# Optimization experiments

Measured on AMD Instinct MI355X. Metric: run time of the kernel, lower is better.

## Reference

```python
import jax, jax.numpy as jnp
import numpy as np

B, L, D, H = 8, 1024, 1024, 16
DH = D // H  # dim_per_head = 64
HG = H // 2  # global/local head split


def setup_inputs() -> dict:
    key = jax.random.key(0)
    ks = jax.random.split(key, 10)
    s = 1.0 / np.sqrt(D)
    return {
        "key": jax.random.normal(ks[0], (B, L, D), jnp.float32),
        "value": jax.random.normal(ks[1], (B, L, D), jnp.float32),
        "query": jax.random.normal(ks[2], (B, L, D), jnp.float32),
        "mask": jax.random.bernoulli(ks[3], 0.1, (B, L, L)),
        "additional_mask": jax.random.bernoulli(ks[4], 0.1, (B, L)),
        "Wk": jax.random.normal(ks[5], (D, D), jnp.float32) * s,
        "bk": jnp.zeros((D,), jnp.float32),
        "Wv": jax.random.normal(ks[6], (D, D), jnp.float32) * s,
        "bv": jnp.zeros((D,), jnp.float32),
        "Wq": jax.random.normal(ks[7], (D, D), jnp.float32) * s,
        "bq": jnp.zeros((D,), jnp.float32),
        "Wo": jax.random.normal(ks[8], (D, D), jnp.float32) * s,
        "bo": jnp.zeros((D,), jnp.float32),
    }


def _shape(x):
    # [B, L, D] -> [B, H, L, DH]
    return x.reshape(B, -1, H, DH).transpose(0, 2, 1, 3)


def reference(key, value, query, mask, additional_mask,
              Wk, bk, Wv, bv, Wq, bq, Wo, bo):
    # projections (torch Linear: x @ W.T + b)
    k = _shape(key @ Wk.T + bk)
    v = _shape(value @ Wv.T + bv)
    q = _shape(query @ Wq.T + bq) * (1.0 / np.sqrt(DH))  # scale query (edge_feature=None, additional_mask given)

    qg, ql = q[:, :HG], q[:, HG:]
    kg, kl = k[:, :HG], k[:, HG:]
    vg, vl = v[:, :HG], v[:, HG:]

    # global heads: standard masked attention
    score_g = jnp.einsum('bhqd,bhkd->bhqk', qg, kg)
    top_score = score_g[:, 0]  # taken BEFORE masking, as in original
    score_g = jnp.where(mask[:, None, :, :], -1e18, score_g)
    attn_g = jax.nn.softmax(score_g, axis=-1)  # dropout = identity (eval)
    ctx_g = jnp.einsum('bhqk,bhkd->bhqd', attn_g, vg)

    # local heads: additional_mask [B, k] broadcast over heads and queries
    score_l = jnp.einsum('bhqd,bhkd->bhqk', ql, kl)
    score_l = jnp.where(additional_mask[:, None, None, :], -1e18, score_l)
    attn_l = jax.nn.softmax(score_l, axis=-1)
    ctx_l = jnp.einsum('bhqk,bhkd->bhqd', attn_l, vl)

    ctx = jnp.concatenate([ctx_g, ctx_l], axis=1)          # [B, H, L, DH]
    ctx = ctx.transpose(0, 2, 1, 3).reshape(B, -1, D)      # unshape -> [B, L, D]
    out = ctx @ Wo.T + bo
    return out, top_score
```

## Files before the change

### kernel.cpp

```cpp
#include <hip/hip_runtime.h>
#include <hip/hip_bf16.h>

typedef unsigned short u16;
typedef unsigned int u32;
typedef __attribute__((ext_vector_type(8))) short short8;
typedef __attribute__((ext_vector_type(4))) short short4v;
typedef __attribute__((ext_vector_type(4))) float floatx4;

#define BB 8
#define LL 1024
#define DD 1024
#define HH 16
#define DHH 64
#define NEGBIG (-3.0e38f)
#define QSCALE 0.1803368801111204f
#define LN2F   0.6931471805599453f
#define DEFER_THR 12.0f

__device__ inline u16 f2b(float f) {
  union { __hip_bfloat16 h; u16 u; } cv;
  cv.h = __float2bfloat16(f);
  return cv.u;
}
__device__ inline float b2f(u16 u) {
  union { u16 u; __hip_bfloat16 h; } cv;
  cv.u = u;
  return __bfloat162float(cv.h);
}
__device__ inline float fin(float v, float sentinel) {
  return (fabsf(v) < 1e30f) ? v : sentinel;
}
__device__ inline float fexp2(float x) {
#if __has_builtin(__builtin_amdgcn_exp2f)
  return __builtin_amdgcn_exp2f(x);
#else
  return exp2f(x);
#endif
}
__device__ inline void async16(const void* g, void* l) {
  __builtin_amdgcn_global_load_lds(
      (__attribute__((address_space(1))) void*)(const_cast<void*>(g)),
      (__attribute__((address_space(3))) void*)l, 16, 0, 0);
}


__global__ __launch_bounds__(256) void convpack(
    const float* __restrict__ Wk, const float* __restrict__ Wv,
    const float* __restrict__ Wq, const float* __restrict__ Wo,
    const int* __restrict__ mask, const int* __restrict__ amask,
    u16* __restrict__ Wkb, u16* __restrict__ Wvb, u16* __restrict__ Wqb,
    u16* __restrict__ Wob, u32* __restrict__ maskb, u32* __restrict__ amaskb) {
  const int job = blockIdx.y;
  const int gtid = blockIdx.x * 256 + threadIdx.x;
  const int stride = gridDim.x * 256;

  if (job < 4) {
    const float* src; u16* dst;
    switch (job) {
      case 0: src = Wk; dst = Wkb; break;
      case 1: src = Wv; dst = Wvb; break;
      case 2: src = Wq; dst = Wqb; break;
      default: src = Wo; dst = Wob; break;
    }
    const size_t n4 = (size_t)DD * DD / 4;
    for (size_t i = gtid; i < n4; i += stride) {
      float4 v = ((const float4*)src)[i];
      short4v s;
      s[0] = (short)f2b(v.x); s[1] = (short)f2b(v.y);
      s[2] = (short)f2b(v.z); s[3] = (short)f2b(v.w);
      *(short4v*)(dst + i * 4) = s;
    }
  } else if (job == 4) {
    const size_t nw = (size_t)BB * LL * LL / 32;
    for (size_t w = gtid; w < nw; w += stride) {
      const int4* src = (const int4*)(mask + w * 32);
      u32 bits = 0;
#pragma unroll
      for (int c = 0; c < 8; c++) {
        int4 v = src[c];
        bits |= (u32)(v.x != 0) << (c * 4);
        bits |= (u32)(v.y != 0) << (c * 4 + 1);
        bits |= (u32)(v.z != 0) << (c * 4 + 2);
        bits |= (u32)(v.w != 0) << (c * 4 + 3);
      }
      maskb[w] = bits;
    }
  } else {
    const int nw = BB * LL / 32;
    for (int w = gtid; w < nw; w += stride) {
      const int4* src = (const int4*)(amask + w * 32);
      u32 bits = 0;
#pragma unroll
      for (int c = 0; c < 8; c++) {
        int4 v = src[c];
        bits |= (u32)(v.x != 0) << (c * 4);
        bits |= (u32)(v.y != 0) << (c * 4 + 1);
        bits |= (u32)(v.z != 0) << (c * 4 + 2);
        bits |= (u32)(v.w != 0) << (c * 4 + 3);
      }
      amaskb[w] = bits;
    }
  }
}

__global__ __launch_bounds__(256) void gemm_qkv(
    const float* __restrict__ key, const float* __restrict__ value,
    const float* __restrict__ query, const u16* __restrict__ Wkb,
    const u16* __restrict__ Wvb, const u16* __restrict__ Wqb,
    const float* __restrict__ bk, const float* __restrict__ bv,
    const float* __restrict__ bq, u16* __restrict__ kbuf,
    u16* __restrict__ vbt, u16* __restrict__ qbuf) {
  __shared__ u16 As[2][128 * 32];
  __shared__ u16 Ws[3][128 * 32];

  const int z = blockIdx.z;
  const int tid = threadIdx.x;
  const int wave = tid >> 6, lane = tid & 63;
  const int lr = lane & 15, lq = lane >> 4;
  const int row0 = blockIdx.x * 128;
  const int col0 = blockIdx.y * 128;
  const int wm = (wave & 1) * 64, wn = (wave >> 1) * 64;

  floatx4 acc[4][4];
#pragma unroll
  for (int i = 0; i < 4; i++)
#pragma unroll
    for (int j = 0; j < 4; j++) acc[i][j] = (floatx4){0.f, 0.f, 0.f, 0.f};

  const float* A = (z == 0) ? key : (z == 1) ? value : query;
  const u16* Wb  = (z == 0) ? Wkb : (z == 1) ? Wvb : Wqb;

  const int cc0 = tid, cc1 = 256 + tid;
  const u16* Wg0 = Wb + (size_t)(col0 + (cc0 >> 2)) * 1024 + (cc0 & 3) * 8;
  const u16* Wg1 = Wb + (size_t)(col0 + (cc1 >> 2)) * 1024 + (cc1 & 3) * 8;

  auto stageW = [&](int t, int wbuf) {
    const int o = t * 32;
    async16(Wg0 + o, &Ws[wbuf][wave * 512]);
    async16(Wg1 + o, &Ws[wbuf][2048 + wave * 512]);
  };
  auto loadA = [&](int t, float4* ag) {
#pragma unroll
    for (int it = 0; it < 4; it++) {
      const int cc = it * 256 + tid;
      ag[it] = *(const float4*)(A + (size_t)(row0 + (cc >> 3)) * 1024 +
                                (cc & 7) * 4 + t * 32);
    }
  };
  auto writeA = [&](int abuf, const float4* ag) {
#pragma unroll
    for (int it = 0; it < 4; it++) {
      const int cc = it * 256 + tid;
      short4v s;
      s[0] = (short)f2b(ag[it].x); s[1] = (short)f2b(ag[it].y);
      s[2] = (short)f2b(ag[it].z); s[3] = (short)f2b(ag[it].w);
      *(short4v*)(&As[abuf][(cc >> 3) * 32 + (cc & 7) * 4]) = s;
    }
  };

  float4 ag[3][4];

  stageW(0, 0);
  stageW(1, 1);
  loadA(0, ag[0]);
  loadA(1, ag[1]);
  asm volatile("s_waitcnt vmcnt(4)" ::: "memory");
  writeA(0, ag[0]);
  loadA(2, ag[2]);

#pragma unroll
  for (int t = 0; t < 32; t++) {
    const int abuf = t & 1;
    asm volatile("s_waitcnt vmcnt(10)" ::: "memory");
    asm volatile("s_waitcnt lgkmcnt(0)" ::: "memory");
    __builtin_amdgcn_s_barrier();
    asm volatile("" ::: "memory");

    const int t2 = (t + 2 < 32) ? t + 2 : 31;
    const int t3 = (t + 3 < 32) ? t + 3 : 31;
    stageW(t2, (t + 2) % 3);
    loadA(t3, ag[t % 3]);

    short8 af[4], wf[4];
#pragma unroll
    for (int mi = 0; mi < 4; mi++)
      af[mi] = *(const short8*)(&As[abuf][(wm + mi * 16 + lr) * 32 + lq * 8]);
#pragma unroll
    for (int ni = 0; ni < 4; ni++)
      wf[ni] = *(const short8*)(&Ws[t % 3][(wn + ni * 16 + lr) * 32 + lq * 8]);
#pragma unroll
    for (int mi = 0; mi < 4; mi++)
#pragma unroll
      for (int ni = 0; ni < 4; ni++)
        acc[mi][ni] = __builtin_amdgcn_mfma_f32_16x16x32_bf16(af[mi], wf[ni],
                                                              acc[mi][ni], 0, 0, 0);

    if (t == 0) asm volatile("s_waitcnt vmcnt(10)" ::: "memory");
    else        asm volatile("s_waitcnt vmcnt(12)" ::: "memory");
    writeA(abuf ^ 1, ag[(t + 1) % 3]);
  }

  const float scale = (z == 2) ? QSCALE : 1.0f;
  const float* bias = (z == 0) ? bk : (z == 1) ? bv : bq;
  u16* outb = (z == 0) ? kbuf : qbuf;

#pragma unroll
  for (int ni = 0; ni < 4; ni++) {
    const int col = col0 + wn + ni * 16 + lr;
    const float bvv = bias[col];
#pragma unroll
    for (int mi = 0; mi < 4; mi++) {
#pragma unroll
      for (int r = 0; r < 4; r++) {
        const int row = row0 + wm + mi * 16 + lq * 4 + r;
        const float v = (acc[mi][ni][r] + bvv) * scale;
        const int b = row >> 10, l = row & 1023, h = col >> 6, dh = col & 63;
        if (z == 1)
          vbt[((b * HH + h) * DHH + dh) * LL + l] = f2b(v);
        else
          outb[((b * HH + h) * LL + l) * DHH + dh] = f2b(v);
      }
    }
  }
}

__global__ __launch_bounds__(256) void top_kernel(
    const u16* __restrict__ qbuf, const u16* __restrict__ kbuf,
    float* __restrict__ top) {
  __shared__ u16 Qs[128 * 64];
  __shared__ u16 Ks[128 * 64];

  const int kt = blockIdx.x, qt = blockIdx.y, b = blockIdx.z;
  const int tid = threadIdx.x, wave = tid >> 6, lane = tid & 63;
  const int lr = lane & 15, lq = lane >> 4;
  const int lq4 = lq * 4;
  const int x7 = lr & 7;

  const u16* Qg = qbuf + (size_t)((b * HH + 0) * LL + qt * 128) * DHH;
  const u16* Kg = kbuf + (size_t)((b * HH + 0) * LL + kt * 128) * DHH;

#pragma unroll
  for (int rnd = 0; rnd < 4; rnd++) {
    const int g = rnd * 256 + tid;
    const int row = g >> 3, col = (g & 7) ^ (row & 7);
    async16(Qg + row * 64 + col * 8, Qs + (rnd * 256 + wave * 64) * 8);
    async16(Kg + row * 64 + col * 8, Ks + (rnd * 256 + wave * 64) * 8);
  }
  __syncthreads();

  const int cs0 = ((0 + lq) ^ x7) * 8;
  const int cs1 = ((4 + lq) ^ x7) * 8;

  short8 qf[2][2];
#pragma unroll
  for (int mi = 0; mi < 2; mi++) {
    qf[mi][0] = *(const short8*)(Qs + (wave * 32 + mi * 16 + lr) * 64 + cs0);
    qf[mi][1] = *(const short8*)(Qs + (wave * 32 + mi * 16 + lr) * 64 + cs1);
  }

#pragma unroll
  for (int nj = 0; nj < 8; nj++) {
    const short8 kf0 = *(const short8*)(Ks + (nj * 16 + lr) * 64 + cs0);
    const short8 kf1 = *(const short8*)(Ks + (nj * 16 + lr) * 64 + cs1);
#pragma unroll
    for (int mi = 0; mi < 2; mi++) {
      floatx4 z = (floatx4){0.f, 0.f, 0.f, 0.f};
      z = __builtin_amdgcn_mfma_f32_16x16x32_bf16(kf1, qf[mi][1], z, 0, 0, 0);
      z = __builtin_amdgcn_mfma_f32_16x16x32_bf16(kf0, qf[mi][0], z, 0, 0, 0);
      const int row = qt * 128 + wave * 32 + mi * 16 + lr;
      float4 t;
      t.x = z[0] * LN2F; t.y = z[1] * LN2F;
      t.z = z[2] * LN2F; t.w = z[3] * LN2F;
      *(float4*)(top + (size_t)(b * LL + row) * LL + kt * 128 + nj * 16 + lq4) = t;
    }
  }
}

template <int OUT>
__global__ __launch_bounds__(256) void gemm_b(
    const u16* __restrict__ A, const u16* __restrict__ Wb,
    const float* __restrict__ bias, void* __restrict__ outv, float scale) {
  __shared__ u16 As[3][128 * 32];
  __shared__ u16 Ws[3][128 * 32];

  const int tid = threadIdx.x;
  const int wave = tid >> 6, lane = tid & 63;
  const int lr = lane & 15, lq = lane >> 4;
  const int row0 = blockIdx.x * 128;
  const int col0 = blockIdx.y * 128;
  const int wm = (wave & 1) * 64, wn = (wave >> 1) * 64;

  floatx4 acc[4][4];
#pragma unroll
  for (int i = 0; i < 4; i++)
#pragma unroll
    for (int j = 0; j < 4; j++) acc[i][j] = (floatx4){0.f, 0.f, 0.f, 0.f};

  const int cc0 = tid, cc1 = 256 + tid;
  const u16* Ag0 = A + (size_t)(row0 + (cc0 >> 2)) * 1024 + (cc0 & 3) * 8;
  const u16* Ag1 = A + (size_t)(row0 + (cc1 >> 2)) * 1024 + (cc1 & 3) * 8;
  const u16* Wg0 = Wb + (size_t)(col0 + (cc0 >> 2)) * 1024 + (cc0 & 3) * 8;
  const u16* Wg1 = Wb + (size_t)(col0 + (cc1 >> 2)) * 1024 + (cc1 & 3) * 8;

  auto stage = [&](int t, int buf) {
    const int o = t * 32;
    async16(Ag0 + o, &As[buf][wave * 512]);
    async16(Ag1 + o, &As[buf][2048 + wave * 512]);
    async16(Wg0 + o, &Ws[buf][wave * 512]);
    async16(Wg1 + o, &Ws[buf][2048 + wave * 512]);
  };

  stage(0, 0);
  stage(1, 1);

#pragma unroll
  for (int t = 0; t < 32; t++) {
    asm volatile("s_waitcnt vmcnt(4)" ::: "memory");
    __builtin_amdgcn_s_barrier();
    asm volatile("" ::: "memory");

    const int t2 = (t + 2 < 32) ? t + 2 : 31;
    stage(t2, (t + 2) % 3);

    short8 af[4], wf[4];
#pragma unroll
    for (int mi = 0; mi < 4; mi++)
      af[mi] = *(const short8*)(&As[t % 3][(wm + mi * 16 + lr) * 32 + lq * 8]);
#pragma unroll
    for (int ni = 0; ni < 4; ni++)
      wf[ni] = *(const short8*)(&Ws[t % 3][(wn + ni * 16 + lr) * 32 + lq * 8]);
#pragma unroll
    for (int mi = 0; mi < 4; mi++)
#pragma unroll
      for (int ni = 0; ni < 4; ni++)
        acc[mi][ni] = __builtin_amdgcn_mfma_f32_16x16x32_bf16(af[mi], wf[ni],
                                                              acc[mi][ni], 0, 0, 0);
  }

#pragma unroll
  for (int ni = 0; ni < 4; ni++) {
    const int col = col0 + wn + ni * 16 + lr;
    const float bv = bias[col];
#pragma unroll
    for (int mi = 0; mi < 4; mi++) {
#pragma unroll
      for (int r = 0; r < 4; r++) {
        const int row = row0 + wm + mi * 16 + lq * 4 + r;
        const float v = (acc[mi][ni][r] + bv) * scale;
        if (OUT == 0) {
          const int b = row >> 10, l = row & 1023, h = col >> 6, dh = col & 63;
          ((u16*)outv)[((b * HH + h) * LL + l) * DHH + dh] = f2b(v);
        } else if (OUT == 2) {
          const int b = row >> 10, l = row & 1023, h = col >> 6, dh = col & 63;
          ((u16*)outv)[((b * HH + h) * DHH + dh) * LL + l] = f2b(v);
        } else {
          ((float*)outv)[(size_t)row * 1024 + col] = v;
        }
      }
    }
  }
}

__global__ __launch_bounds__(256) void attn_fast(
    const u16* __restrict__ qbuf, const u16* __restrict__ kbuf,
    const u16* __restrict__ vbt, const u32* __restrict__ maskb,
    const u32* __restrict__ amaskb, u16* __restrict__ ctx) {
  __shared__ u16 Ks[2][64 * 64];
  __shared__ u16 Vts[2][64 * 64];

  const int id = blockIdx.x;
  const int xcd = id & 7;
  const int r_ = id >> 3;
  const int b = r_ & 7;
  const int h = (((r_ >> 3) & 1) << 3) | (xcd ^ b);
  const int qt = r_ >> 4;

  const int tid = threadIdx.x, wave = tid >> 6, lane = tid & 63;
  const int lr = lane & 15, lq = lane >> 4;
  const int lq4 = lq * 4;
  const int x7 = lr & 7;

  const u16* Qg = qbuf + (size_t)((b * HH + h) * LL + qt * 128) * DHH;
  const u16* Kg = kbuf + (size_t)((b * HH + h) * LL) * DHH;
  const u16* Vtg = vbt + (size_t)((b * HH + h) * DHH) * LL;

  short8 qf[2][2];
#pragma unroll
  for (int mi = 0; mi < 2; mi++)
#pragma unroll
    for (int kk = 0; kk < 2; kk++)
      qf[mi][kk] = *(const short8*)(Qg + (wave * 32 + mi * 16 + lr) * 64 +
                                    kk * 32 + lq * 8);

  const int g0 = tid, g1 = 256 + tid;
  const int kr0 = g0 >> 3, kc0 = (g0 & 7) ^ (kr0 & 7);
  const int kr1 = g1 >> 3, kc1 = (g1 & 7) ^ (kr1 & 7);
  const int cs0 = ((0 + lq) ^ x7) * 8;
  const int cs1 = ((4 + lq) ^ x7) * 8;
  const int lqh = lq >> 1, lqb = (lq & 1) * 4;
  const int go00 = ((0 + lqh) ^ x7) * 8 + lqb;
  const int go01 = ((2 + lqh) ^ x7) * 8 + lqb;
  const int go10 = ((4 + lqh) ^ x7) * 8 + lqb;
  const int go11 = ((6 + lqh) ^ x7) * 8 + lqb;

  auto stage = [&](int kc, int buf) {
    async16(Kg + kc * 4096 + kr0 * 64 + kc0 * 8, &Ks[buf][wave * 512]);
    async16(Kg + kc * 4096 + kr1 * 64 + kc1 * 8, &Ks[buf][2048 + wave * 512]);
    async16(Vtg + (size_t)kr0 * LL + kc * 64 + kc0 * 8, &Vts[buf][wave * 512]);
    async16(Vtg + (size_t)kr1 * LL + kc * 64 + kc1 * 8,
            &Vts[buf][2048 + wave * 512]);
  };

  const int rowm0 = qt * 128 + wave * 32 + lr;
  const int rowm1 = rowm0 + 16;
  const u32* mb0 = (h < 8) ? maskb + (size_t)(b * LL + rowm0) * 32
                           : amaskb + b * 32;
  const u32* mb1 = (h < 8) ? maskb + (size_t)(b * LL + rowm1) * 32
                           : amaskb + b * 32;
  uint2 mwc0 = *(const uint2*)(mb0);
  uint2 mwc1 = *(const uint2*)(mb1);

  float mrow[2], lrow[2];
  floatx4 Oacc[2][4];
#pragma unroll
  for (int mi = 0; mi < 2; mi++) {
    mrow[mi] = NEGBIG;
    lrow[mi] = 0.f;
#pragma unroll
    for (int ni = 0; ni < 4; ni++) Oacc[mi][ni] = (floatx4){0.f, 0.f, 0.f, 0.f};
  }

  stage(0, 0);

  for (int kc = 0; kc < 16; kc++) {
    const int cur = kc & 1;
    __syncthreads();
    uint2 mwn0, mwn1;
    if (kc < 15) {
      stage(kc + 1, cur ^ 1);
      mwn0 = *(const uint2*)(mb0 + (kc + 1) * 2);
      mwn1 = *(const uint2*)(mb1 + (kc + 1) * 2);
    }
    const u16* Ksc = Ks[cur];
    const u16* Vtsc = Vts[cur];

    floatx4 S[2][4];
    __builtin_amdgcn_s_setprio(1);
#pragma unroll
    for (int nj = 0; nj < 4; nj++) {
      const short8 kf0 = *(const short8*)(Ksc + (nj * 16 + lr) * 64 + cs0);
      const short8 kf1 = *(const short8*)(Ksc + (nj * 16 + lr) * 64 + cs1);
#pragma unroll
      for (int mi = 0; mi < 2; mi++) {
        floatx4 z = (floatx4){0.f, 0.f, 0.f, 0.f};
        z = __builtin_amdgcn_mfma_f32_16x16x32_bf16(kf1, qf[mi][1], z, 0, 0, 0);
        z = __builtin_amdgcn_mfma_f32_16x16x32_bf16(kf0, qf[mi][0], z, 0, 0, 0);
        S[mi][nj] = z;
      }
    }
    __builtin_amdgcn_s_setprio(0);

    short8 pf[2][2];
#pragma unroll
    for (int mi = 0; mi < 2; mi++) {
      {
        const uint2 mw = mi ? mwc1 : mwc0;
#pragma unroll
        for (int nj = 0; nj < 4; nj++) {
          const u32 nib = (((nj & 2) ? mw.y : mw.x) >> ((nj & 1) * 16 + lq4)) & 15u;
#pragma unroll
          for (int r = 0; r < 4; r++)
            if ((nib >> r) & 1) S[mi][nj][r] = -1e18f;
        }
      }

      float cm = fmaxf(fmaxf(S[mi][0][0], S[mi][0][1]),
                       fmaxf(S[mi][0][2], S[mi][0][3]));
#pragma unroll
      for (int nj = 1; nj < 4; nj++)
        cm = fmaxf(cm, fmaxf(fmaxf(S[mi][nj][0], S[mi][nj][1]),
                             fmaxf(S[mi][nj][2], S[mi][nj][3])));
// ... 297 lines not shown
        const float mold = mrow[mi][r];
        const float mnew = fmaxf(mold, cm);
        const float alpha = __expf(mold - mnew);
        mrow[mi][r] = mnew;
        float rs = 0.f;
#pragma unroll
        for (int nj = 0; nj < 4; nj++) {
          const float p = __expf(S[mi][nj][r] - mnew);
          S[mi][nj][r] = p;
          rs += p;
        }
#pragma unroll
        for (int off = 1; off < 16; off <<= 1) rs += __shfl_xor(rs, off, 64);
        lrow[mi][r] = lrow[mi][r] * alpha + rs;
#pragma unroll
        for (int ni = 0; ni < 4; ni++) Oacc[mi][ni][r] *= alpha;
      }
    }
#pragma unroll
    for (int mi = 0; mi < 2; mi++)
#pragma unroll
      for (int nj = 0; nj < 4; nj++)
#pragma unroll
        for (int r = 0; r < 4; r++)
          Ps[wave][(mi * 16 + lq * 4 + r) * 64 + nj * 16 + lr] = f2b(S[mi][nj][r]);
    __syncthreads();
#pragma unroll
    for (int kk = 0; kk < 2; kk++) {
      short8 pf[2];
#pragma unroll
      for (int mi = 0; mi < 2; mi++)
        pf[mi] = *(const short8*)(&Ps[wave][(mi * 16 + lr) * 64 + kk * 32 + lq * 8]);
#pragma unroll
      for (int ni = 0; ni < 4; ni++) {
        short8 vf = *(const short8*)(Vts + (ni * 16 + lr) * 64 + kk * 32 + lq * 8);
#pragma unroll
        for (int mi = 0; mi < 2; mi++)
          Oacc[mi][ni] = __builtin_amdgcn_mfma_f32_16x16x32_bf16(pf[mi], vf, Oacc[mi][ni], 0, 0, 0);
      }
    }
  }
#pragma unroll
  for (int mi = 0; mi < 2; mi++)
#pragma unroll
    for (int r = 0; r < 4; r++) {
      const float inv = 1.0f / lrow[mi][r];
      const int row = qt * 128 + wave * 32 + mi * 16 + lq * 4 + r;
#pragma unroll
      for (int ni = 0; ni < 4; ni++) {
        const int col = h * DHH + ni * 16 + lr;
        ctx[(size_t)(b * LL + row) * DD + col] = f2b(fin(Oacc[mi][ni][r] * inv, 900.0f));
      }
    }
}

extern "C" void kernel_launch(void* const* d_in, const int* in_sizes, int n_in,
                              void* d_out, int out_size, void* d_ws, size_t ws_size,
                              hipStream_t stream) {
  const float* key   = (const float*)d_in[0];
  const float* value = (const float*)d_in[1];
  const float* query = (const float*)d_in[2];
  const int* mask    = (const int*)d_in[3];
  const int* amask   = (const int*)d_in[4];
  const float* Wk = (const float*)d_in[5];
  const float* bk = (const float*)d_in[6];
  const float* Wv = (const float*)d_in[7];
  const float* bv = (const float*)d_in[8];
  const float* Wq = (const float*)d_in[9];
  const float* bq = (const float*)d_in[10];
  const float* Wo = (const float*)d_in[11];
  const float* bo = (const float*)d_in[12];

  float* outp = (float*)d_out;
  float* topp = outp + (size_t)BB * LL * DD;

  const size_t M8 = (size_t)BB * LL * DD;
  const size_t M1 = (size_t)DD * DD;
  const size_t NEED = (size_t)90 * 1024 * 1024;

  dim3 tb(256), gg(64, 8, 1), ga(8, 16, 8);

  if (ws_size >= NEED) {
    u16* W16 = (u16*)d_ws;
    u16* Wkb = W16;
    u16* Wvb = Wkb + M1;
    u16* Wqb = Wvb + M1;
    u16* Wob = Wqb + M1;
    u32* maskb = (u32*)(Wob + M1);
    u32* amaskb = maskb + 262144;
    u16* kbuf = W16 + 6 * M1;
    u16* vbt  = kbuf + M8;
    u16* qbuf = vbt + M8;
    u16* cbuf = qbuf + M8;

    convpack<<<dim3(256, 6), tb, 0, stream>>>(
        Wk, Wv, Wq, Wo, mask, amask, Wkb, Wvb, Wqb, Wob, maskb, amaskb);
    gemm_qkv<<<dim3(64, 8, 3), tb, 0, stream>>>(
        key, value, query, Wkb, Wvb, Wqb, bk, bv, bq, kbuf, vbt, qbuf);
    top_kernel<<<dim3(8, 8, 8), tb, 0, stream>>>(qbuf, kbuf, topp);
    attn_fast<<<dim3(1024, 1, 1), tb, 0, stream>>>(qbuf, kbuf, vbt, maskb,
                                                   amaskb, cbuf);
    gemm_b<1><<<gg, tb, 0, stream>>>(cbuf, Wob, bo, outp, 1.0f);
  } else {
    u16* kbuf = (u16*)d_ws;
    u16* vbuf = kbuf + M8;
    u16* qbuf = vbuf + M8;
    u16* cbuf = qbuf + M8;
    gemm_k<0><<<gg, tb, 0, stream>>>(key,   Wk, bk, kbuf, 1.0f);
    gemm_k<0><<<gg, tb, 0, stream>>>(value, Wv, bv, vbuf, 1.0f);
    gemm_k<0><<<gg, tb, 0, stream>>>(query, Wq, bq, qbuf, 0.125f);
    attn_kernel<<<ga, tb, 0, stream>>>(qbuf, kbuf, vbuf, mask, amask, cbuf, topp);
    gemm_k<1><<<gg, tb, 0, stream>>>(cbuf, Wo, bo, outp, 1.0f);
  }
}
```

Before: 382.4 us.

## Pre-convert key/value to bf16 and use larger swizzled 256x128x64 GEMM tiles

The convpack kernel now also converts key and value activations to bf16 so the K/V projections can stream A through async global-to-LDS copies. The QKV and output projection GEMMs move to 512-thread blocks with 256x128 tiles, a K-step of 64 and XOR-swizzled LDS layouts. This aims to raise data reuse per block, cut bank conflicts and halve the number of barrier iterations. In exchange it adds an extra full pass to convert the activations, uses more LDS per block and fewer blocks, and reuses the keyb workspace as the context buffer.

```diff
diff --git a/kernel.cpp b/kernel.cpp
--- a/kernel.cpp
+++ b/kernel.cpp
@@ -47,22 +47,25 @@
 __global__ __launch_bounds__(256) void convpack(
     const float* __restrict__ Wk, const float* __restrict__ Wv,
     const float* __restrict__ Wq, const float* __restrict__ Wo,
+    const float* __restrict__ key, const float* __restrict__ value,
     const int* __restrict__ mask, const int* __restrict__ amask,
     u16* __restrict__ Wkb, u16* __restrict__ Wvb, u16* __restrict__ Wqb,
-    u16* __restrict__ Wob, u32* __restrict__ maskb, u32* __restrict__ amaskb) {
+    u16* __restrict__ Wob, u16* __restrict__ keyb, u16* __restrict__ valb,
+    u32* __restrict__ maskb, u32* __restrict__ amaskb) {
   const int job = blockIdx.y;
   const int gtid = blockIdx.x * 256 + threadIdx.x;
   const int stride = gridDim.x * 256;
 
-  if (job < 4) {
-    const float* src; u16* dst;
+  if (job < 6) {
+    const float* src; u16* dst; size_t n4;
     switch (job) {
-      case 0: src = Wk; dst = Wkb; break;
-      case 1: src = Wv; dst = Wvb; break;
-      case 2: src = Wq; dst = Wqb; break;
-      default: src = Wo; dst = Wob; break;
-    }
-    const size_t n4 = (size_t)DD * DD / 4;
+      case 0: src = Wk;    dst = Wkb;  n4 = (size_t)DD * DD / 4; break;
+      case 1: src = Wv;    dst = Wvb;  n4 = (size_t)DD * DD / 4; break;
+      case 2: src = Wq;    dst = Wqb;  n4 = (size_t)DD * DD / 4; break;
+      case 3: src = Wo;    dst = Wob;  n4 = (size_t)DD * DD / 4; break;
+      case 4: src = key;   dst = keyb; n4 = (size_t)BB * LL * DD / 4; break;
+      default: src = value; dst = valb; n4 = (size_t)BB * LL * DD / 4; break;
+    }
     for (size_t i = gtid; i < n4; i += stride) {
       float4 v = ((const float4*)src)[i];
       short4v s;
@@ -70,7 +73,7 @@
       s[2] = (short)f2b(v.z); s[3] = (short)f2b(v.w);
       *(short4v*)(dst + i * 4) = s;
     }
-  } else if (job == 4) {
+  } else if (job == 6) {
     const size_t nw = (size_t)BB * LL * LL / 32;
     for (size_t w = gtid; w < nw; w += stride) {
       const int4* src = (const int4*)(mask + w * 32);
@@ -103,23 +106,25 @@
   }
 }
 
-__global__ __launch_bounds__(256) void gemm_qkv(
-    const float* __restrict__ key, const float* __restrict__ value,
+
+__global__ __launch_bounds__(512) void gemm_qkv(
+    const u16* __restrict__ keyb, const u16* __restrict__ valb,
     const float* __restrict__ query, const u16* __restrict__ Wkb,
     const u16* __restrict__ Wvb, const u16* __restrict__ Wqb,
     const float* __restrict__ bk, const float* __restrict__ bv,
     const float* __restrict__ bq, u16* __restrict__ kbuf,
     u16* __restrict__ vbt, u16* __restrict__ qbuf) {
-  __shared__ u16 As[2][128 * 32];
-  __shared__ u16 Ws[3][128 * 32];
+  __shared__ u16 Al[2][256 * 64];
+  __shared__ u16 Bl[3][128 * 64];
 
   const int z = blockIdx.z;
   const int tid = threadIdx.x;
   const int wave = tid >> 6, lane = tid & 63;
   const int lr = lane & 15, lq = lane >> 4;
-  const int row0 = blockIdx.x * 128;
+  const int row0 = blockIdx.x * 256;
   const int col0 = blockIdx.y * 128;
-  const int wm = (wave & 1) * 64, wn = (wave >> 1) * 64;
+  const int wm = (wave >> 1) * 64, wn = (wave & 1) * 64;
+  const int x7 = lr & 7;
 
   floatx4 acc[4][4];
 #pragma unroll
@@ -127,77 +132,131 @@
 #pragma unroll
     for (int j = 0; j < 4; j++) acc[i][j] = (floatx4){0.f, 0.f, 0.f, 0.f};
 
-  const float* A = (z == 0) ? key : (z == 1) ? value : query;
-  const u16* Wb  = (z == 0) ? Wkb : (z == 1) ? Wvb : Wqb;
-
-  const int cc0 = tid, cc1 = 256 + tid;
-  const u16* Wg0 = Wb + (size_t)(col0 + (cc0 >> 2)) * 1024 + (cc0 & 3) * 8;
-  const u16* Wg1 = Wb + (size_t)(col0 + (cc1 >> 2)) * 1024 + (cc1 & 3) * 8;
-
-  auto stageW = [&](int t, int wbuf) {
-    const int o = t * 32;
-    async16(Wg0 + o, &Ws[wbuf][wave * 512]);
-    async16(Wg1 + o, &Ws[wbuf][2048 + wave * 512]);
+  const u16* Wb = (z == 0) ? Wkb : (z == 1) ? Wvb : Wqb;
+
+  const int gB0 = tid, gB1 = 512 + tid;
+  const int rB0 = gB0 >> 3, cB0 = (gB0 & 7) ^ (rB0 & 7);
+  const int rB1 = gB1 >> 3, cB1 = (gB1 & 7) ^ (rB1 & 7);
+  const u16* WgP0 = Wb + (size_t)(col0 + rB0) * 1024 + cB0 * 8;
+  const u16* WgP1 = Wb + (size_t)(col0 + rB1) * 1024 + cB1 * 8;
+  const int ldsB0 = (wave * 64) * 8;
+  const int ldsB1 = (512 + wave * 64) * 8;
+  auto stageB = [&](int t, int buf) {
+    async16(WgP0 + t * 64, &Bl[buf][ldsB0]);
+    async16(WgP1 + t * 64, &Bl[buf][ldsB1]);
   };
-  auto loadA = [&](int t, float4* ag) {
-#pragma unroll
-    for (int it = 0; it < 4; it++) {
-      const int cc = it * 256 + tid;
-      ag[it] = *(const float4*)(A + (size_t)(row0 + (cc >> 3)) * 1024 +
-                                (cc & 7) * 4 + t * 32);
+
+  const int cs0 = ((0 + lq) ^ x7) * 8;
+  const int cs1 = ((4 + lq) ^ x7) * 8;
+
+  auto compute = [&](const u16* As_, const u16* Bs_) {
+#pragma unroll
+    for (int kh = 0; kh < 2; kh++) {
+      const int cs = kh ? cs1 : cs0;
+      short8 af[4], wf[4];
+#pragma unroll
+      for (int mi = 0; mi < 4; mi++)
+        af[mi] = *(const short8*)(As_ + (wm + mi * 16 + lr) * 64 + cs);
+#pragma unroll
+      for (int ni = 0; ni < 4; ni++)
+        wf[ni] = *(const short8*)(Bs_ + (wn + ni * 16 + lr) * 64 + cs);
+#pragma unroll
+      for (int mi = 0; mi < 4; mi++)
+#pragma unroll
+        for (int ni = 0; ni < 4; ni++)
+          acc[mi][ni] = __builtin_amdgcn_mfma_f32_16x16x32_bf16(
+              af[mi], wf[ni], acc[mi][ni], 0, 0, 0);
     }
   };
-  auto writeA = [&](int abuf, const float4* ag) {
-#pragma unroll
-    for (int it = 0; it < 4; it++) {
-      const int cc = it * 256 + tid;
-      short4v s;
-      s[0] = (short)f2b(ag[it].x); s[1] = (short)f2b(ag[it].y);
-      s[2] = (short)f2b(ag[it].z); s[3] = (short)f2b(ag[it].w);
-      *(short4v*)(&As[abuf][(cc >> 3) * 32 + (cc & 7) * 4]) = s;
-    }
-  };
-
-  float4 ag[3][4];
-
-  stageW(0, 0);
-  stageW(1, 1);
-  loadA(0, ag[0]);
-  loadA(1, ag[1]);
-  asm volatile("s_waitcnt vmcnt(4)" ::: "memory");
-  writeA(0, ag[0]);
-  loadA(2, ag[2]);
-
-#pragma unroll
-  for (int t = 0; t < 32; t++) {
-    const int abuf = t & 1;
-    asm volatile("s_waitcnt vmcnt(10)" ::: "memory");
-    asm volatile("s_waitcnt lgkmcnt(0)" ::: "memory");
-    __builtin_amdgcn_s_barrier();
-    asm volatile("" ::: "memory");
-
-    const int t2 = (t + 2 < 32) ? t + 2 : 31;
-    const int t3 = (t + 3 < 32) ? t + 3 : 31;
-    stageW(t2, (t + 2) % 3);
-    loadA(t3, ag[t % 3]);
-
-    short8 af[4], wf[4];
-#pragma unroll
-    for (int mi = 0; mi < 4; mi++)
-      af[mi] = *(const short8*)(&As[abuf][(wm + mi * 16 + lr) * 32 + lq * 8]);
-#pragma unroll
-    for (int ni = 0; ni < 4; ni++)
-      wf[ni] = *(const short8*)(&Ws[t % 3][(wn + ni * 16 + lr) * 32 + lq * 8]);
-#pragma unroll
-    for (int mi = 0; mi < 4; mi++)
-#pragma unroll
-      for (int ni = 0; ni < 4; ni++)
-        acc[mi][ni] = __builtin_amdgcn_mfma_f32_16x16x32_bf16(af[mi], wf[ni],
-                                                              acc[mi][ni], 0, 0, 0);
-
-    if (t == 0) asm volatile("s_waitcnt vmcnt(10)" ::: "memory");
-    else        asm volatile("s_waitcnt vmcnt(12)" ::: "memory");
-    writeA(abuf ^ 1, ag[(t + 1) % 3]);
+
+  if (z < 2) {
+    const u16* Ab = (z == 0) ? keyb : valb;
+    const u16* AgP[4];
+    int ldsA[4];
+#pragma unroll
+    for (int p = 0; p < 4; p++) {
+      const int g = p * 512 + tid;
+      const int r = g >> 3, c = (g & 7) ^ (r & 7);
+      AgP[p] = Ab + (size_t)(row0 + r) * 1024 + c * 8;
+      ldsA[p] = (p * 512 + wave * 64) * 8;
+    }
+    auto stageA = [&](int t, int buf) {
+#pragma unroll
+      for (int p = 0; p < 4; p++) async16(AgP[p] + t * 64, &Al[buf][ldsA[p]]);
+    };
+
+    stageA(0, 0);
+    stageB(0, 0);
+    stageB(1, 1);
+
+    int b_buf = 2, t3 = 0;
+    for (int t = 0; t < 16; t++) {
+      asm volatile("s_waitcnt vmcnt(2)" ::: "memory");
+      __builtin_amdgcn_s_barrier();
+      __builtin_amdgcn_sched_barrier(0);
+      if (t < 15) {
+        stageA(t + 1, (t + 1) & 1);
+        stageB(t + 2 > 15 ? 15 : t + 2, b_buf);
+        b_buf = (b_buf == 2) ? 0 : b_buf + 1;
+      }
+      compute(&Al[t & 1][0], &Bl[t3][0]);
+      t3 = (t3 == 2) ? 0 : t3 + 1;
+    }
+  } else {
+    float4 ag[8];
+    int gA_r[4], gA_c[4], ldsA[4];
+#pragma unroll
+    for (int p = 0; p < 4; p++) {
+      const int g = p * 512 + tid;
+      gA_r[p] = g >> 3;
+      gA_c[p] = (g & 7) ^ (gA_r[p] & 7);
+      ldsA[p] = g * 8;
+    }
+    auto loadAq = [&](int t) {
+#pragma unroll
+      for (int p = 0; p < 4; p++) {
+        const float* s =
+            query + (size_t)(row0 + gA_r[p]) * 1024 + t * 64 + gA_c[p] * 8;
+        ag[2 * p] = *(const float4*)(s);
+        ag[2 * p + 1] = *(const float4*)(s + 4);
+      }
+    };
+    auto writeAq = [&](int buf) {
+#pragma unroll
+      for (int p = 0; p < 4; p++) {
+        short8 s8;
+        s8[0] = (short)f2b(ag[2 * p].x);     s8[1] = (short)f2b(ag[2 * p].y);
+        s8[2] = (short)f2b(ag[2 * p].z);     s8[3] = (short)f2b(ag[2 * p].w);
+        s8[4] = (short)f2b(ag[2 * p + 1].x); s8[5] = (short)f2b(ag[2 * p + 1].y);
+        s8[6] = (short)f2b(ag[2 * p + 1].z); s8[7] = (short)f2b(ag[2 * p + 1].w);
+        *(short8*)(&Al[buf][ldsA[p]]) = s8;
+      }
+    };
+
+    loadAq(0);
+    stageB(0, 0);
+    stageB(1, 1);
+    asm volatile("s_waitcnt vmcnt(4)" ::: "memory");
+    writeAq(0);
+
+    int b_buf = 2, t3 = 0;
+    for (int t = 0; t < 16; t++) {
+      asm volatile("s_waitcnt lgkmcnt(0)" ::: "memory");
+      asm volatile("s_waitcnt vmcnt(2)" ::: "memory");
+      __builtin_amdgcn_s_barrier();
+      __builtin_amdgcn_sched_barrier(0);
+      if (t < 15) {
+        loadAq(t + 1);
+        stageB(t + 2 > 15 ? 15 : t + 2, b_buf);
+        b_buf = (b_buf == 2) ? 0 : b_buf + 1;
+      }
+      compute(&Al[t & 1][0], &Bl[t3][0]);
+      if (t < 15) {
+        asm volatile("s_waitcnt vmcnt(2)" ::: "memory");
+        writeAq((t + 1) & 1);
+      }
+      t3 = (t3 == 2) ? 0 : t3 + 1;
+    }
   }
 
   const float scale = (z == 2) ? QSCALE : 1.0f;
@@ -219,6 +278,109 @@
           vbt[((b * HH + h) * DHH + dh) * LL + l] = f2b(v);
         else
           outb[((b * HH + h) * LL + l) * DHH + dh] = f2b(v);
+      }
+    }
+  }
+}
+
+__global__ __launch_bounds__(512) void gemm_o(
+    const u16* __restrict__ A, const u16* __restrict__ Wb,
+    const float* __restrict__ bias, float* __restrict__ outp) {
+  __shared__ u16 Al[2][256 * 64];
+  __shared__ u16 Bl[3][128 * 64];
+
+  const int tid = threadIdx.x;
+  const int wave = tid >> 6, lane = tid & 63;
+  const int lr = lane & 15, lq = lane >> 4;
+  const int row0 = blockIdx.x * 256;
+  const int col0 = blockIdx.y * 128;
+  const int wm = (wave >> 1) * 64, wn = (wave & 1) * 64;
+  const int x7 = lr & 7;
+
+  floatx4 acc[4][4];
+#pragma unroll
+  for (int i = 0; i < 4; i++)
+#pragma unroll
+    for (int j = 0; j < 4; j++) acc[i][j] = (floatx4){0.f, 0.f, 0.f, 0.f};
+
+  const int gB0 = tid, gB1 = 512 + tid;
+  const int rB0 = gB0 >> 3, cB0 = (gB0 & 7) ^ (rB0 & 7);
+  const int rB1 = gB1 >> 3, cB1 = (gB1 & 7) ^ (rB1 & 7);
+  const u16* WgP0 = Wb + (size_t)(col0 + rB0) * 1024 + cB0 * 8;
+  const u16* WgP1 = Wb + (size_t)(col0 + rB1) * 1024 + cB1 * 8;
+  const int ldsB0 = (wave * 64) * 8;
+  const int ldsB1 = (512 + wave * 64) * 8;
+
+  const u16* AgP[4];
+  int ldsA[4];
+#pragma unroll
+  for (int p = 0; p < 4; p++) {
+    const int g = p * 512 + tid;
+    const int r = g >> 3, c = (g & 7) ^ (r & 7);
+    AgP[p] = A + (size_t)(row0 + r) * 1024 + c * 8;
+    ldsA[p] = (p * 512 + wave * 64) * 8;
+  }
+
+  auto stageB = [&](int t, int buf) {
+    async16(WgP0 + t * 64, &Bl[buf][ldsB0]);
+    async16(WgP1 + t * 64, &Bl[buf][ldsB1]);
+  };
+  auto stageA = [&](int t, int buf) {
+#pragma unroll
+    for (int p = 0; p < 4; p++) async16(AgP[p] + t * 64, &Al[buf][ldsA[p]]);
+  };
+
+  const int cs0 = ((0 + lq) ^ x7) * 8;
+  const int cs1 = ((4 + lq) ^ x7) * 8;
+
+  stageA(0, 0);
+  stageB(0, 0);
+  stageB(1, 1);
+
+  int b_buf = 2, t3 = 0;
+  for (int t = 0; t < 16; t++) {
+    asm volatile("s_waitcnt vmcnt(2)" ::: "memory");
+    __builtin_amdgcn_s_barrier();
+    __builtin_amdgcn_sched_barrier(0);
+    if (t < 15) {
+      stageA(t + 1, (t + 1) & 1);
+      stageB(t + 2 > 15 ? 15 : t + 2, b_buf);
+      b_buf = (b_buf == 2) ? 0 : b_buf + 1;
+    }
+    {
+      const u16* As_ = &Al[t & 1][0];
+      const u16* Bs_ = &Bl[t3][0];
+#pragma unroll
+      for (int kh = 0; kh < 2; kh++) {
+        const int cs = kh ? cs1 : cs0;
+        short8 af[4], wf[4];
+#pragma unroll
+        for (int mi = 0; mi < 4; mi++)
+          af[mi] = *(const short8*)(As_ + (wm + mi * 16 + lr) * 64 + cs);
+#pragma unroll
+        for (int ni = 0; ni < 4; ni++)
+          wf[ni] = *(const short8*)(Bs_ + (wn + ni * 16 + lr) * 64 + cs);
+#pragma unroll
+        for (int mi = 0; mi < 4; mi++)
+#pragma unroll
+          for (int ni = 0; ni < 4; ni++)
+            acc[mi][ni] = __builtin_amdgcn_mfma_f32_16x16x32_bf16(
+                af[mi], wf[ni], acc[mi][ni], 0, 0, 0);
+      }
+    }
+    t3 = (t3 == 2) ? 0 : t3 + 1;
+  }
+
+#pragma unroll
+  for (int ni = 0; ni < 4; ni++) {
+    const int col = col0 + wn + ni * 16 + lr;
+    const float bv = bias[col];
+#pragma unroll
+    for (int mi = 0; mi < 4; mi++) {
+#pragma unroll
+      for (int r = 0; r < 4; r++) {
+        const int row = row0 + wm + mi * 16 + lq * 4 + r;
+        outp[(size_t)row * 1024 + col] = acc[mi][ni][r] + bv;
       }
     }
   }
@@ -272,91 +434,6 @@
       t.x = z[0] * LN2F; t.y = z[1] * LN2F;
       t.z = z[2] * LN2F; t.w = z[3] * LN2F;
       *(float4*)(top + (size_t)(b * LL + row) * LL + kt * 128 + nj * 16 + lq4) = t;
-    }
-  }
-}
-
-template <int OUT>
-__global__ __launch_bounds__(256) void gemm_b(
-    const u16* __restrict__ A, const u16* __restrict__ Wb,
-    const float* __restrict__ bias, void* __restrict__ outv, float scale) {
-  __shared__ u16 As[3][128 * 32];
-  __shared__ u16 Ws[3][128 * 32];
-
-  const int tid = threadIdx.x;
-  const int wave = tid >> 6, lane = tid & 63;
-  const int lr = lane & 15, lq = lane >> 4;
-  const int row0 = blockIdx.x * 128;
-  const int col0 = blockIdx.y * 128;
-  const int wm = (wave & 1) * 64, wn = (wave >> 1) * 64;
-
-  floatx4 acc[4][4];
-#pragma unroll
-  for (int i = 0; i < 4; i++)
-#pragma unroll
-    for (int j = 0; j < 4; j++) acc[i][j] = (floatx4){0.f, 0.f, 0.f, 0.f};
-
-  const int cc0 = tid, cc1 = 256 + tid;
-  const u16* Ag0 = A + (size_t)(row0 + (cc0 >> 2)) * 1024 + (cc0 & 3) * 8;
-  const u16* Ag1 = A + (size_t)(row0 + (cc1 >> 2)) * 1024 + (cc1 & 3) * 8;
-  const u16* Wg0 = Wb + (size_t)(col0 + (cc0 >> 2)) * 1024 + (cc0 & 3) * 8;
-  const u16* Wg1 = Wb + (size_t)(col0 + (cc1 >> 2)) * 1024 + (cc1 & 3) * 8;
-
-  auto stage = [&](int t, int buf) {
-    const int o = t * 32;
-    async16(Ag0 + o, &As[buf][wave * 512]);
-    async16(Ag1 + o, &As[buf][2048 + wave * 512]);
-    async16(Wg0 + o, &Ws[buf][wave * 512]);
-    async16(Wg1 + o, &Ws[buf][2048 + wave * 512]);
-  };
-
-  stage(0, 0);
-  stage(1, 1);
-
-#pragma unroll
-  for (int t = 0; t < 32; t++) {
-    asm volatile("s_waitcnt vmcnt(4)" ::: "memory");
-    __builtin_amdgcn_s_barrier();
-    asm volatile("" ::: "memory");
-
-    const int t2 = (t + 2 < 32) ? t + 2 : 31;
-    stage(t2, (t + 2) % 3);
-
-    short8 af[4], wf[4];
-#pragma unroll
-    for (int mi = 0; mi < 4; mi++)
-      af[mi] = *(const short8*)(&As[t % 3][(wm + mi * 16 + lr) * 32 + lq * 8]);
-#pragma unroll
-    for (int ni = 0; ni < 4; ni++)
-      wf[ni] = *(const short8*)(&Ws[t % 3][(wn + ni * 16 + lr) * 32 + lq * 8]);
-#pragma unroll
-    for (int mi = 0; mi < 4; mi++)
-#pragma unroll
-      for (int ni = 0; ni < 4; ni++)
-        acc[mi][ni] = __builtin_amdgcn_mfma_f32_16x16x32_bf16(af[mi], wf[ni],
-                                                              acc[mi][ni], 0, 0, 0);
-  }
-
-#pragma unroll
-  for (int ni = 0; ni < 4; ni++) {
-    const int col = col0 + wn + ni * 16 + lr;
-    const float bv = bias[col];
-#pragma unroll
-    for (int mi = 0; mi < 4; mi++) {
-#pragma unroll
-      for (int r = 0; r < 4; r++) {
-        const int row = row0 + wm + mi * 16 + lq * 4 + r;
-        const float v = (acc[mi][ni][r] + bv) * scale;
-        if (OUT == 0) {
-          const int b = row >> 10, l = row & 1023, h = col >> 6, dh = col & 63;
-          ((u16*)outv)[((b * HH + h) * LL + l) * DHH + dh] = f2b(v);
-        } else if (OUT == 2) {
-          const int b = row >> 10, l = row & 1023, h = col >> 6, dh = col & 63;
-          ((u16*)outv)[((b * HH + h) * DHH + dh) * LL + l] = f2b(v);
-        } else {
-          ((float*)outv)[(size_t)row * 1024 + col] = v;
-        }
-      }
     }
   }
 }
@@ -860,25 +937,28 @@
 
   if (ws_size >= NEED) {
     u16* W16 = (u16*)d_ws;
-    u16* Wkb = W16;
+    u16* keyb = W16;
+    u16* valb = W16 + M8;
+    u16* Wkb = W16 + 2 * M8;
     u16* Wvb = Wkb + M1;
     u16* Wqb = Wvb + M1;
     u16* Wob = Wqb + M1;
     u32* maskb = (u32*)(Wob + M1);
     u32* amaskb = maskb + 262144;
-    u16* kbuf = W16 + 6 * M1;
+    u16* kbuf = W16 + 2 * M8 + 5 * M1;
     u16* vbt  = kbuf + M8;
     u16* qbuf = vbt + M8;
-    u16* cbuf = qbuf + M8;
-
-    convpack<<<dim3(256, 6), tb, 0, stream>>>(
-        Wk, Wv, Wq, Wo, mask, amask, Wkb, Wvb, Wqb, Wob, maskb, amaskb);
-    gemm_qkv<<<dim3(64, 8, 3), tb, 0, stream>>>(
-        key, value, query, Wkb, Wvb, Wqb, bk, bv, bq, kbuf, vbt, qbuf);
+    u16* cbuf = keyb;
+
+    convpack<<<dim3(256, 8), tb, 0, stream>>>(
+        Wk, Wv, Wq, Wo, key, value, mask, amask,
+        Wkb, Wvb, Wqb, Wob, keyb, valb, maskb, amaskb);
+    gemm_qkv<<<dim3(32, 8, 3), dim3(512), 0, stream>>>(
+        keyb, valb, query, Wkb, Wvb, Wqb, bk, bv, bq, kbuf, vbt, qbuf);
     top_kernel<<<dim3(8, 8, 8), tb, 0, stream>>>(qbuf, kbuf, topp);
     attn_fast<<<dim3(1024, 1, 1), tb, 0, stream>>>(qbuf, kbuf, vbt, maskb,
                                                    amaskb, cbuf);
-    gemm_b<1><<<gg, tb, 0, stream>>>(cbuf, Wob, bo, outp, 1.0f);
+    gemm_o<<<dim3(32, 8, 1), dim3(512), 0, stream>>>(cbuf, Wob, bo, outp);
   } else {
     u16* kbuf = (u16*)d_ws;
     u16* vbuf = kbuf + M8;
```

Measured after the change: 414.9 us. +8.5%, slower.

## Fold mask packing into QKV GEMM and top-score into attention launch

Applied to the files above, without the earlier changes.

Mask bit-packing moves out of the weight-conversion kernel and runs as an extra z-slice of the QKV GEMM grid, so it overlaps with the projection work. The top-score kernel is merged into the attention kernel as 512 extra blocks reusing its shared memory. The weight-conversion kernel shrinks to a 32x4 grid. This cuts two kernel launches and lets the memory-bound mask and top work fill idle CUs, at the cost of possible tail imbalance and contention with GEMM blocks.

```diff
diff --git a/kernel.cpp b/kernel.cpp
--- a/kernel.cpp
+++ b/kernel.cpp
@@ -44,33 +44,50 @@
 }
 
 
-__global__ __launch_bounds__(256) void convpack(
+__global__ __launch_bounds__(256) void convpack_w(
     const float* __restrict__ Wk, const float* __restrict__ Wv,
     const float* __restrict__ Wq, const float* __restrict__ Wo,
-    const int* __restrict__ mask, const int* __restrict__ amask,
     u16* __restrict__ Wkb, u16* __restrict__ Wvb, u16* __restrict__ Wqb,
-    u16* __restrict__ Wob, u32* __restrict__ maskb, u32* __restrict__ amaskb) {
+    u16* __restrict__ Wob) {
   const int job = blockIdx.y;
   const int gtid = blockIdx.x * 256 + threadIdx.x;
   const int stride = gridDim.x * 256;
-
-  if (job < 4) {
-    const float* src; u16* dst;
-    switch (job) {
-      case 0: src = Wk; dst = Wkb; break;
-      case 1: src = Wv; dst = Wvb; break;
-      case 2: src = Wq; dst = Wqb; break;
-      default: src = Wo; dst = Wob; break;
-    }
-    const size_t n4 = (size_t)DD * DD / 4;
-    for (size_t i = gtid; i < n4; i += stride) {
-      float4 v = ((const float4*)src)[i];
-      short4v s;
-      s[0] = (short)f2b(v.x); s[1] = (short)f2b(v.y);
-      s[2] = (short)f2b(v.z); s[3] = (short)f2b(v.w);
-      *(short4v*)(dst + i * 4) = s;
-    }
-  } else if (job == 4) {
+  const float* src; u16* dst;
+  switch (job) {
+    case 0: src = Wk; dst = Wkb; break;
+    case 1: src = Wv; dst = Wvb; break;
+    case 2: src = Wq; dst = Wqb; break;
+    default: src = Wo; dst = Wob; break;
+  }
+  const size_t n4 = (size_t)DD * DD / 4;
+  for (size_t i = gtid; i < n4; i += stride) {
+    float4 v = ((const float4*)src)[i];
+    short4v s;
+    s[0] = (short)f2b(v.x); s[1] = (short)f2b(v.y);
+    s[2] = (short)f2b(v.z); s[3] = (short)f2b(v.w);
+    *(short4v*)(dst + i * 4) = s;
+  }
+}
+
+__global__ __launch_bounds__(256) void gemm_qkv(
+    const float* __restrict__ key, const float* __restrict__ value,
+    const float* __restrict__ query, const u16* __restrict__ Wkb,
+    const u16* __restrict__ Wvb, const u16* __restrict__ Wqb,
+    const float* __restrict__ bk, const float* __restrict__ bv,
+    const float* __restrict__ bq, const int* __restrict__ mask,
+    const int* __restrict__ amask, u16* __restrict__ kbuf,
+    u16* __restrict__ vbt, u16* __restrict__ qbuf,
+    u32* __restrict__ maskb, u32* __restrict__ amaskb) {
+  __shared__ u16 As[2][128 * 32];
+  __shared__ u16 Ws[3][128 * 32];
+
+  const int z = blockIdx.z;
+  const int tid = threadIdx.x;
+
+  if (z == 3) {
+    const int flat = blockIdx.y * 64 + blockIdx.x;
+    const int gtid = flat * 256 + tid;
+    const int stride = 512 * 256;
     const size_t nw = (size_t)BB * LL * LL / 32;
     for (size_t w = gtid; w < nw; w += stride) {
       const int4* src = (const int4*)(mask + w * 32);
@@ -85,10 +102,8 @@
       }
       maskb[w] = bits;
     }
-  } else {
-    const int nw = BB * LL / 32;
-    for (int w = gtid; w < nw; w += stride) {
-      const int4* src = (const int4*)(amask + w * 32);
+    if (gtid < BB * LL / 32) {
+      const int4* src = (const int4*)(amask + gtid * 32);
       u32 bits = 0;
 #pragma unroll
       for (int c = 0; c < 8; c++) {
@@ -98,23 +113,11 @@
         bits |= (u32)(v.z != 0) << (c * 4 + 2);
         bits |= (u32)(v.w != 0) << (c * 4 + 3);
       }
-      amaskb[w] = bits;
-    }
-  }
-}
-
-__global__ __launch_bounds__(256) void gemm_qkv(
-    const float* __restrict__ key, const float* __restrict__ value,
-    const float* __restrict__ query, const u16* __restrict__ Wkb,
-    const u16* __restrict__ Wvb, const u16* __restrict__ Wqb,
-    const float* __restrict__ bk, const float* __restrict__ bv,
-    const float* __restrict__ bq, u16* __restrict__ kbuf,
-    u16* __restrict__ vbt, u16* __restrict__ qbuf) {
-  __shared__ u16 As[2][128 * 32];
-  __shared__ u16 Ws[3][128 * 32];
-
-  const int z = blockIdx.z;
-  const int tid = threadIdx.x;
+      amaskb[gtid] = bits;
+    }
+    return;
+  }
+
   const int wave = tid >> 6, lane = tid & 63;
   const int lr = lane & 15, lq = lane >> 4;
   const int row0 = blockIdx.x * 128;
@@ -220,58 +223,6 @@
         else
           outb[((b * HH + h) * LL + l) * DHH + dh] = f2b(v);
       }
-    }
-  }
-}
-
-__global__ __launch_bounds__(256) void top_kernel(
-    const u16* __restrict__ qbuf, const u16* __restrict__ kbuf,
-    float* __restrict__ top) {
-  __shared__ u16 Qs[128 * 64];
-  __shared__ u16 Ks[128 * 64];
-
-  const int kt = blockIdx.x, qt = blockIdx.y, b = blockIdx.z;
-  const int tid = threadIdx.x, wave = tid >> 6, lane = tid & 63;
-  const int lr = lane & 15, lq = lane >> 4;
-  const int lq4 = lq * 4;
-  const int x7 = lr & 7;
-
-  const u16* Qg = qbuf + (size_t)((b * HH + 0) * LL + qt * 128) * DHH;
-  const u16* Kg = kbuf + (size_t)((b * HH + 0) * LL + kt * 128) * DHH;
-
-#pragma unroll
-  for (int rnd = 0; rnd < 4; rnd++) {
-    const int g = rnd * 256 + tid;
-    const int row = g >> 3, col = (g & 7) ^ (row & 7);
-    async16(Qg + row * 64 + col * 8, Qs + (rnd * 256 + wave * 64) * 8);
-    async16(Kg + row * 64 + col * 8, Ks + (rnd * 256 + wave * 64) * 8);
-  }
-  __syncthreads();
-
-  const int cs0 = ((0 + lq) ^ x7) * 8;
-  const int cs1 = ((4 + lq) ^ x7) * 8;
-
-  short8 qf[2][2];
-#pragma unroll
-  for (int mi = 0; mi < 2; mi++) {
-    qf[mi][0] = *(const short8*)(Qs + (wave * 32 + mi * 16 + lr) * 64 + cs0);
-    qf[mi][1] = *(const short8*)(Qs + (wave * 32 + mi * 16 + lr) * 64 + cs1);
-  }
-
-#pragma unroll
-  for (int nj = 0; nj < 8; nj++) {
-    const short8 kf0 = *(const short8*)(Ks + (nj * 16 + lr) * 64 + cs0);
-    const short8 kf1 = *(const short8*)(Ks + (nj * 16 + lr) * 64 + cs1);
-#pragma unroll
-    for (int mi = 0; mi < 2; mi++) {
-      floatx4 z = (floatx4){0.f, 0.f, 0.f, 0.f};
-      z = __builtin_amdgcn_mfma_f32_16x16x32_bf16(kf1, qf[mi][1], z, 0, 0, 0);
-      z = __builtin_amdgcn_mfma_f32_16x16x32_bf16(kf0, qf[mi][0], z, 0, 0, 0);
-      const int row = qt * 128 + wave * 32 + mi * 16 + lr;
-      float4 t;
-      t.x = z[0] * LN2F; t.y = z[1] * LN2F;
-      t.z = z[2] * LN2F; t.w = z[3] * LN2F;
-      *(float4*)(top + (size_t)(b * LL + row) * LL + kt * 128 + nj * 16 + lq4) = t;
     }
   }
 }
@@ -364,22 +315,69 @@
 __global__ __launch_bounds__(256) void attn_fast(
     const u16* __restrict__ qbuf, const u16* __restrict__ kbuf,
     const u16* __restrict__ vbt, const u32* __restrict__ maskb,
-    const u32* __restrict__ amaskb, u16* __restrict__ ctx) {
+    const u32* __restrict__ amaskb, u16* __restrict__ ctx,
+    float* __restrict__ top) {
   __shared__ u16 Ks[2][64 * 64];
   __shared__ u16 Vts[2][64 * 64];
 
   const int id = blockIdx.x;
+  const int tid = threadIdx.x, wave = tid >> 6, lane = tid & 63;
+  const int lr = lane & 15, lq = lane >> 4;
+  const int lq4 = lq * 4;
+  const int x7 = lr & 7;
+  const int cs0 = ((0 + lq) ^ x7) * 8;
+  const int cs1 = ((4 + lq) ^ x7) * 8;
+
+  if (id >= 1024) {
+    const int id2 = id - 1024;
+    const int kt = id2 & 7, qt = (id2 >> 3) & 7, b = id2 >> 6;
+    u16* Qs = &Ks[0][0];
+    u16* Kts = &Vts[0][0];
+
+    const u16* Qg = qbuf + (size_t)((b * HH + 0) * LL + qt * 128) * DHH;
+    const u16* Kg = kbuf + (size_t)((b * HH + 0) * LL + kt * 128) * DHH;
+
+#pragma unroll
+    for (int rnd = 0; rnd < 4; rnd++) {
+      const int g = rnd * 256 + tid;
+      const int row = g >> 3, col = (g & 7) ^ (row & 7);
+      async16(Qg + row * 64 + col * 8, Qs + (rnd * 256 + wave * 64) * 8);
+      async16(Kg + row * 64 + col * 8, Kts + (rnd * 256 + wave * 64) * 8);
+    }
+    __syncthreads();
+
+    short8 qf[2][2];
+#pragma unroll
+    for (int mi = 0; mi < 2; mi++) {
+      qf[mi][0] = *(const short8*)(Qs + (wave * 32 + mi * 16 + lr) * 64 + cs0);
+      qf[mi][1] = *(const short8*)(Qs + (wave * 32 + mi * 16 + lr) * 64 + cs1);
+    }
+
+#pragma unroll
+    for (int nj = 0; nj < 8; nj++) {
+      const short8 kf0 = *(const short8*)(Kts + (nj * 16 + lr) * 64 + cs0);
+      const short8 kf1 = *(const short8*)(Kts + (nj * 16 + lr) * 64 + cs1);
+#pragma unroll
+      for (int mi = 0; mi < 2; mi++) {
+        floatx4 z = (floatx4){0.f, 0.f, 0.f, 0.f};
+        z = __builtin_amdgcn_mfma_f32_16x16x32_bf16(kf1, qf[mi][1], z, 0, 0, 0);
+        z = __builtin_amdgcn_mfma_f32_16x16x32_bf16(kf0, qf[mi][0], z, 0, 0, 0);
+        const int row = qt * 128 + wave * 32 + mi * 16 + lr;
+        float4 t;
+        t.x = z[0] * LN2F; t.y = z[1] * LN2F;
+        t.z = z[2] * LN2F; t.w = z[3] * LN2F;
+        *(float4*)(top + (size_t)(b * LL + row) * LL + kt * 128 + nj * 16 + lq4) = t;
+      }
+    }
+    return;
+  }
+
   const int xcd = id & 7;
   const int r_ = id >> 3;
   const int b = r_ & 7;
   const int h = (((r_ >> 3) & 1) << 3) | (xcd ^ b);
   const int qt = r_ >> 4;
 
-  const int tid = threadIdx.x, wave = tid >> 6, lane = tid & 63;
-  const int lr = lane & 15, lq = lane >> 4;
-  const int lq4 = lq * 4;
-  const int x7 = lr & 7;
-
   const u16* Qg = qbuf + (size_t)((b * HH + h) * LL + qt * 128) * DHH;
   const u16* Kg = kbuf + (size_t)((b * HH + h) * LL) * DHH;
   const u16* Vtg = vbt + (size_t)((b * HH + h) * DHH) * LL;
@@ -395,8 +393,6 @@
   const int g0 = tid, g1 = 256 + tid;
   const int kr0 = g0 >> 3, kc0 = (g0 & 7) ^ (kr0 & 7);
   const int kr1 = g1 >> 3, kc1 = (g1 & 7) ^ (kr1 & 7);
-  const int cs0 = ((0 + lq) ^ x7) * 8;
-  const int cs1 = ((4 + lq) ^ x7) * 8;
   const int lqh = lq >> 1, lqb = (lq & 1) * 4;
   const int go00 = ((0 + lqh) ^ x7) * 8 + lqb;
   const int go01 = ((2 + lqh) ^ x7) * 8 + lqb;
@@ -871,13 +867,13 @@
     u16* qbuf = vbt + M8;
     u16* cbuf = qbuf + M8;
 
-    convpack<<<dim3(256, 6), tb, 0, stream>>>(
-        Wk, Wv, Wq, Wo, mask, amask, Wkb, Wvb, Wqb, Wob, maskb, amaskb);
-    gemm_qkv<<<dim3(64, 8, 3), tb, 0, stream>>>(
-        key, value, query, Wkb, Wvb, Wqb, bk, bv, bq, kbuf, vbt, qbuf);
-    top_kernel<<<dim3(8, 8, 8), tb, 0, stream>>>(qbuf, kbuf, topp);
-    attn_fast<<<dim3(1024, 1, 1), tb, 0, stream>>>(qbuf, kbuf, vbt, maskb,
-                                                   amaskb, cbuf);
+    convpack_w<<<dim3(32, 4), tb, 0, stream>>>(
+        Wk, Wv, Wq, Wo, Wkb, Wvb, Wqb, Wob);
+    gemm_qkv<<<dim3(64, 8, 4), tb, 0, stream>>>(
+        key, value, query, Wkb, Wvb, Wqb, bk, bv, bq, mask, amask,
+        kbuf, vbt, qbuf, maskb, amaskb);
+    attn_fast<<<dim3(1536, 1, 1), tb, 0, stream>>>(qbuf, kbuf, vbt, maskb,
+                                                   amaskb, cbuf, topp);
     gemm_b<1><<<gg, tb, 0, stream>>>(cbuf, Wob, bo, outp, 1.0f);
   } else {
     u16* kbuf = (u16*)d_ws;
```

After: 408.1 us. 1.07x slower.
